# Kernel tuning notes

Hardware: AMD Instinct MI355X
Metric: run time of the kernel (lower is better)

The kernel has to match this reference:

```python
import jax, jax.numpy as jnp
import numpy as np

N = 50000      # nodes
E = 800000     # edges (avg degree 16)
F_IN = 64      # node_feature_dim
D = 128        # hidden_dim == output_dim
L = 3          # num_gnn_layers
B = 8          # number of graphs in the batch
GATE_H = 128   # GraphAttentionPool hidden_dim default


def _ln(x, g, b, eps=1e-5):
    m = x.mean(-1, keepdims=True)
    v = ((x - m) ** 2).mean(-1, keepdims=True)
    return (x - m) * jax.lax.rsqrt(v + eps) * g + b


def _gelu(x):
    return jax.nn.gelu(x, approximate=False)  # torch F.gelu default = exact erf


def setup_inputs() -> dict:
    key = jax.random.key(0)
    ks = jax.random.split(key, 12)
    p = lambda k, shape: (jax.random.normal(k, shape, jnp.float32) * 0.02)
    return {
        "x": jax.random.normal(ks[0], (N, F_IN), jnp.float32),
        "edge_index": jax.random.randint(ks[1], (2, E), 0, N, dtype=jnp.int32),
        "batch": jnp.sort(jax.random.randint(ks[2], (N,), 0, B, dtype=jnp.int32)),
        # input_proj: Linear + LayerNorm
        "w_in": p(ks[3], (F_IN, D)), "b_in": jnp.zeros((D,), jnp.float32),
        "ln_in_g": jnp.ones((D,), jnp.float32), "ln_in_b": jnp.zeros((D,), jnp.float32),
        # fallback GNN layers (stacked: all layers are 2D -> D)
        "gnn_w": p(ks[4], (L, 2 * D, D)), "gnn_b": jnp.zeros((L, D), jnp.float32),
        "gnn_ln_g": jnp.ones((L, D), jnp.float32), "gnn_ln_b": jnp.zeros((L, D), jnp.float32),
        # outer per-layer norms
        "norm_g": jnp.ones((L, D), jnp.float32), "norm_b": jnp.zeros((L, D), jnp.float32),
        # attention pool gate: Linear(D,128) -> tanh -> Linear(128,1)
        "gate_w1": p(ks[5], (D, GATE_H)), "gate_b1": jnp.zeros((GATE_H,), jnp.float32),
        "gate_w2": p(ks[6], (GATE_H,)), "gate_b2": jnp.zeros((), jnp.float32),
        # out_proj: Linear + LayerNorm + GELU
        "out_w": p(ks[7], (D, D)), "out_b": jnp.zeros((D,), jnp.float32),
        "out_ln_g": jnp.ones((D,), jnp.float32), "out_ln_b": jnp.zeros((D,), jnp.float32),
    }


def reference(x, edge_index, batch, w_in, b_in, ln_in_g, ln_in_b,
              gnn_w, gnn_b, gnn_ln_g, gnn_ln_b, norm_g, norm_b,
              gate_w1, gate_b1, gate_w2, gate_b2,
              out_w, out_b, out_ln_g, out_ln_b):
    src, dst = edge_index[0], edge_index[1]
    n = x.shape[0]

    # input_proj: Linear -> LayerNorm -> GELU
    h = _gelu(_ln(x @ w_in + b_in, ln_in_g, ln_in_b))

    # in-degree count (same every layer), clamped to >= 1
    deg = jax.ops.segment_sum(jnp.ones((src.shape[0],), h.dtype), dst, num_segments=n)
    deg = jnp.maximum(deg, 1.0)[:, None]  # (N, 1)

    for i in range(L):
        # mean-neighbor aggregation: gather x[src], scatter-add to dst
        agg = jax.ops.segment_sum(h[src], dst, num_segments=n) / deg  # (N, D)
        out = jnp.concatenate([h, agg], axis=-1) @ gnn_w[i] + gnn_b[i]
        h_new = _ln(_gelu(out), gnn_ln_g[i], gnn_ln_b[i])   # layer-internal norm
        h_new = _ln(h_new, norm_g[i], norm_b[i])             # outer norm
        if i < L - 1:
            h_new = _gelu(h_new) + h                         # residual (shapes match)
        h = h_new

    # attention pool (fallback path: global softmax over all nodes)
    gate_logits = jnp.tanh(h @ gate_w1 + gate_b1) @ gate_w2 + gate_b2  # (N,)
    gate = jax.nn.softmax(gate_logits, axis=0)
    pooled = jax.ops.segment_sum(h * gate[:, None], batch, num_segments=B)  # (B, D)

    spatial_embedding = _gelu(_ln(pooled @ out_w + out_b, out_ln_g, out_ln_b))
    return spatial_embedding, h, gate
```

## Files before the change

kernel.cpp:

```cpp
#include <hip/hip_runtime.h>
#include <math.h>

#define N_NODES 50000
#define N_EDGES 800000
#define F_IN 64
#define D 128
#define NLAYER 3
#define B_GRAPHS 8
#define GB 32
#define NPW 8
#define NBLK ((N_NODES + GB - 1) / GB)
#define SCAN_B 512
#define NPART ((N_NODES + SCAN_B - 1) / SCAN_B)
#define AGP 136

typedef float f32x4 __attribute__((ext_vector_type(4)));
typedef short bf16x8 __attribute__((ext_vector_type(8)));

__device__ __forceinline__ float gelu_exact(float x) {
    return 0.5f * x * (1.0f + erff(x * 0.7071067811865476f));
}

__device__ __forceinline__ unsigned short f2bf(float f) {
    unsigned int u = __float_as_uint(f);
    u = (u + 0x7fffu + ((u >> 16) & 1u)) >> 16;
    return (unsigned short)u;
}
__device__ __forceinline__ float bf2f(unsigned short u) {
    return __uint_as_float((unsigned int)u << 16);
}


__global__ void degree_kernel(const int* __restrict__ dst, int* __restrict__ deg) {
    int e = blockIdx.x * blockDim.x + threadIdx.x;
    if (e < N_EDGES) atomicAdd(&deg[dst[e]], 1);
}

__global__ __launch_bounds__(SCAN_B) void scan_partials_kernel(const int* __restrict__ deg,
                                                               int* __restrict__ partials) {
    __shared__ int wsum[8];
    int tid = threadIdx.x;
    int lane = tid & 63, wave = tid >> 6;
    int i = blockIdx.x * SCAN_B + tid;
    int v = (i < N_NODES) ? deg[i] : 0;
    #pragma unroll
    for (int o = 32; o >= 1; o >>= 1) v += __shfl_xor(v, o);
    if (lane == 0) wsum[wave] = v;
    __syncthreads();
    if (tid == 0) {
        int t = 0;
        #pragma unroll
        for (int w = 0; w < 8; ++w) t += wsum[w];
        partials[blockIdx.x] = t;
    }
}

__global__ __launch_bounds__(SCAN_B) void scan_apply_v2(const int* __restrict__ deg,
        const int* __restrict__ partials, int* __restrict__ row_ptr, int* __restrict__ cursor) {
    __shared__ int wsum[8];
    __shared__ int base_s;
    int tid = threadIdx.x;
    int lane = tid & 63, wave = tid >> 6;

    int b = 0;
    for (int i = tid; i < (int)blockIdx.x; i += SCAN_B) b += partials[i];
    #pragma unroll
    for (int o = 32; o >= 1; o >>= 1) b += __shfl_xor(b, o);
    if (lane == 0) wsum[wave] = b;
    __syncthreads();
    if (tid == 0) {
        int t = 0;
        #pragma unroll
        for (int w = 0; w < 8; ++w) t += wsum[w];
        base_s = t;
    }
    __syncthreads();
    int base = base_s;
    __syncthreads();

    if (blockIdx.x == 0) {
        int t = 0;
        for (int i = tid; i < NPART; i += SCAN_B) t += partials[i];
        #pragma unroll
        for (int o = 32; o >= 1; o >>= 1) t += __shfl_xor(t, o);
        if (lane == 0) wsum[wave] = t;
        __syncthreads();
        if (tid == 0) {
            int tt = 0;
            #pragma unroll
            for (int w = 0; w < 8; ++w) tt += wsum[w];
            row_ptr[N_NODES] = tt;
        }
        __syncthreads();
    }

    int i = blockIdx.x * SCAN_B + tid;
    int v = (i < N_NODES) ? deg[i] : 0;
    int x = v;
    #pragma unroll
    for (int o = 1; o < 64; o <<= 1) { int nb = __shfl_up(x, o); if (lane >= o) x += nb; }
    if (lane == 63) wsum[wave] = x;
    __syncthreads();
    int waveoff = 0;
    #pragma unroll
    for (int w = 0; w < 8; ++w) waveoff += (w < wave) ? wsum[w] : 0;
    int excl = base + waveoff + x - v;
    if (i < N_NODES) { row_ptr[i] = excl; cursor[i] = excl; }
}

__global__ void fill_kernel(const int* __restrict__ src, const int* __restrict__ dst,
                            int* __restrict__ cursor, int* __restrict__ csr) {
    int e = blockIdx.x * blockDim.x + threadIdx.x;
    if (e < N_EDGES) {
        int t = dst[e];
        int pos = atomicAdd(&cursor[t], 1);
        csr[pos] = src[e];
    }
}

#define WT_GNN (NLAYER * D * 2 * D)
#define WT_G1  (WT_GNN + D * D)
#define WT_ALL (WT_G1 + D * F_IN)
__global__ void wprep_kernel(const float* __restrict__ gnn_w, const float* __restrict__ gate_w1,
                             const float* __restrict__ w_in, unsigned short* __restrict__ wt,
                             float* __restrict__ pooled) {
    int idx = blockIdx.x * 256 + threadIdx.x;
    if (blockIdx.x == 0) {
        #pragma unroll
        for (int i = 0; i < 4; ++i) pooled[threadIdx.x + i * 256] = 0.f;
    }
    if (idx >= WT_ALL) return;
    if (idx < WT_GNN) {
        int l = idx / (D * 2 * D);
        int rem = idx - l * (D * 2 * D);
        int n = rem / (2 * D);
        int k = rem - n * (2 * D);
        wt[idx] = f2bf(gnn_w[(size_t)l * 2 * D * D + (size_t)k * D + n]);
    } else if (idx < WT_G1) {
        int rem = idx - WT_GNN;
        int n = rem / D;
        int k = rem - n * D;
        wt[idx] = f2bf(gate_w1[(size_t)k * D + n]);
    } else {
        int rem = idx - WT_G1;
        int n = rem / F_IN;
        int k = rem - n * F_IN;
        wt[idx] = f2bf(w_in[(size_t)k * D + n]);
    }
}


__global__ __launch_bounds__(256) void input_proj_v5(
        const float* __restrict__ x, const unsigned short* __restrict__ wti,
        const float* __restrict__ b, const float* __restrict__ gam,
        const float* __restrict__ bet, unsigned short* __restrict__ h16) {
    __shared__ float2 red[2][GB];
    int tid = threadIdx.x;
    int wave = tid >> 6, lane = tid & 63;
    int nblk0 = blockIdx.x * GB;
    int q = lane >> 4, c = lane & 15;
    int m0 = (wave >> 1) * 16;
    int n0 = (wave & 1) * 64;
    int mrow = nblk0 + m0 + c;
    int mclamp = (mrow < N_NODES) ? mrow : (N_NODES - 1);
    const float* xr = x + (size_t)mclamp * F_IN;

    f32x4 acc[4];
    #pragma unroll
    for (int t = 0; t < 4; ++t) {
        float bn = b[n0 + t * 16 + c];
        acc[t] = (f32x4){bn, bn, bn, bn};
    }
    #pragma unroll
    for (int kk = 0; kk < 2; ++kk) {
        float4 a0 = *(const float4*)&xr[kk * 32 + q * 8];
        float4 a1 = *(const float4*)&xr[kk * 32 + q * 8 + 4];
        bf16x8 av;
        av[0] = (short)f2bf(a0.x); av[1] = (short)f2bf(a0.y);
        av[2] = (short)f2bf(a0.z); av[3] = (short)f2bf(a0.w);
        av[4] = (short)f2bf(a1.x); av[5] = (short)f2bf(a1.y);
        av[6] = (short)f2bf(a1.z); av[7] = (short)f2bf(a1.w);
        #pragma unroll
        for (int t = 0; t < 4; ++t) {
            bf16x8 bv = *(const bf16x8*)&wti[(size_t)(n0 + t * 16 + c) * F_IN + kk * 32 + q * 8];
            acc[t] = __builtin_amdgcn_mfma_f32_16x16x32_bf16(av, bv, acc[t], 0, 0, 0);
        }
    }
    float s[4], sq[4];
    #pragma unroll
    for (int r = 0; r < 4; ++r) {
        s[r] = acc[0][r] + acc[1][r] + acc[2][r] + acc[3][r];
        sq[r] = acc[0][r] * acc[0][r] + acc[1][r] * acc[1][r]
              + acc[2][r] * acc[2][r] + acc[3][r] * acc[3][r];
    }
    #pragma unroll
    for (int o = 1; o <= 8; o <<= 1)
        #pragma unroll
        for (int r = 0; r < 4; ++r) { s[r] += __shfl_xor(s[r], o); sq[r] += __shfl_xor(sq[r], o); }
    if (c == 0) {
        #pragma unroll
        for (int r = 0; r < 4; ++r) red[wave & 1][m0 + q * 4 + r] = make_float2(s[r], sq[r]);
    }
    __syncthreads();
    float gv[4], bv2[4];
    #pragma unroll
    for (int t = 0; t < 4; ++t) {
        int nn = n0 + t * 16 + c;
        gv[t] = gam[nn]; bv2[t] = bet[nn];
    }
    #pragma unroll
    for (int r = 0; r < 4; ++r) {
        int m = m0 + q * 4 + r;
        int n = nblk0 + m;
        float2 p0 = red[0][m], p1 = red[1][m];
        float mean = (p0.x + p1.x) * (1.0f / D);
        float msq  = (p0.y + p1.y) * (1.0f / D);
        float istd = rsqrtf(msq - mean * mean + 1e-5f);
        if (n < N_NODES) {
            #pragma unroll
            for (int t = 0; t < 4; ++t) {
                int nn = n0 + t * 16 + c;
                float y = (acc[t][r] - mean) * istd * gv[t] + bv2[t];
                h16[(size_t)n * D + nn] = f2bf(gelu_exact(y));
            }
        }
    }
}


__device__ __forceinline__ void acc_row(float acc[8], bf16x8 v) {
    #pragma unroll
    for (int i = 0; i < 8; ++i)
        acc[i] += __uint_as_float(((unsigned int)(unsigned short)v[i]) << 16);
}

template<int DO_GATE>
__global__ __launch_bounds__(256) void gnn_layer_v8(
        const unsigned short* __restrict__ h16_in, unsigned short* __restrict__ h16_out,
        float* __restrict__ hf_out,
        const int* __restrict__ csr, const int* __restrict__ rp,
        const unsigned short* __restrict__ wt,
        const float* __restrict__ bias,
        const float* __restrict__ ln1g, const float* __restrict__ ln1b,
        const float* __restrict__ ln2g, const float* __restrict__ ln2b,
        int residual, int write_f32,
        const unsigned short* __restrict__ wtg,
        const float* __restrict__ gb1, const float* __restrict__ gw2,
        const float* __restrict__ gb2,
        float* __restrict__ logits, float2* __restrict__ gpart) {
    __shared__ int rps[GB + 1];
    __shared__ int eidx[GB][32];
    __shared__ unsigned short aggb[GB][AGP];
    __shared__ float2 red1[2][GB];
    __shared__ float2 red2[2][GB];
    __shared__ float redg[2][GB];
    __shared__ float lg[GB];

    int tid = threadIdx.x;
    int wave = tid >> 6, lane = tid & 63;
    int nblk0 = blockIdx.x * GB;
    int gbase = wave * NPW;

    if (tid < GB + 1) {
        int n = nblk0 + tid;
        if (n > N_NODES) n = N_NODES;
        rps[tid] = rp[n];
    }
    __syncthreads();
    #pragma unroll
    for (int k2 = 0; k2 < 4; ++k2) {
        int f = tid + k2 * 256;
        int g = f >> 5, sl = f & 31;
        int beg = rps[g], end = rps[g + 1];
        int ee = beg + sl;
        int ci = (ee < end) ? ee : ((end > beg) ? (end - 1) : 0);
        eidx[g][sl] = csr[ci];
    }
    __syncthreads();

    {
        int er = lane >> 4, dg = lane & 15;
        #pragma unroll
        for (int jj = 0; jj < NPW; jj += 2) {
            int gA = gbase + jj, gB2 = gbase + jj + 1;
            int begA = rps[gA], endA = rps[gA + 1];
            int begB = rps[gB2], endB = rps[gB2 + 1];
            int degA = endA - begA, degB = endB - begB;
            int idA[8], idB[8];
            #pragma unroll
            for (int t = 0; t < 8; ++t) { idA[t] = eidx[gA][er + 4 * t]; idB[t] = eidx[gB2][er + 4 * t]; }
            bf16x8 vA[8], vB[8];
            #pragma unroll
            for (int t = 0; t < 8; ++t)
                vA[t] = *(const bf16x8*)&h16_in[(size_t)idA[t] * D + dg * 8];
            #pragma unroll
            for (int t = 0; t < 8; ++t)
                vB[t] = *(const bf16x8*)&h16_in[(size_t)idB[t] * D + dg * 8];

            float accA[8], accB[8];
            #pragma unroll
            for (int i = 0; i < 8; ++i) { accA[i] = 0.f; accB[i] = 0.f; }
            #pragma unroll
            for (int t = 0; t < 8; ++t)
                if (begA + er + 4 * t < endA) acc_row(accA, vA[t]);
            #pragma unroll
            for (int t = 0; t < 8; ++t)
                if (begB + er + 4 * t < endB) acc_row(accB, vB[t]);
            if (degA > 32) {
                for (int ee = begA + er + 32; ee < endA; ee += 4) {
                    bf16x8 vv = *(const bf16x8*)&h16_in[(size_t)csr[ee] * D + dg * 8];
                    acc_row(accA, vv);
                }
            }
            if (degB > 32) {
                for (int ee = begB + er + 32; ee < endB; ee += 4) {
                    bf16x8 vv = *(const bf16x8*)&h16_in[(size_t)csr[ee] * D + dg * 8];
                    acc_row(accB, vv);
                }
            }
            #pragma unroll
            for (int i = 0; i < 8; ++i) {
                accA[i] += __shfl_xor(accA[i], 16);
                accA[i] += __shfl_xor(accA[i], 32);
                accB[i] += __shfl_xor(accB[i], 16);
                accB[i] += __shfl_xor(accB[i], 32);
            }
            float invA = 1.0f / fmaxf((float)degA, 1.0f);
            float invB = 1.0f / fmaxf((float)degB, 1.0f);
            if (er == 0) {
                bf16x8 oA, oB;
                #pragma unroll
                for (int i = 0; i < 8; ++i) {
                    oA[i] = (short)f2bf(accA[i] * invA);
                    oB[i] = (short)f2bf(accB[i] * invB);
                }
                *(bf16x8*)&aggb[gA][dg * 8] = oA;
                *(bf16x8*)&aggb[gB2][dg * 8] = oB;
            }
        }
    }
    __syncthreads();

    int q = lane >> 4, c = lane & 15;
    int m0 = (wave >> 1) * 16;
    int n0 = (wave & 1) * 64;
    int mrow = nblk0 + m0 + c;
    int mclamp = (mrow < N_NODES) ? mrow : (N_NODES - 1);
    const unsigned short* arow = h16_in + (size_t)mclamp * D;

    f32x4 acc[4];
    #pragma unroll
    for (int t = 0; t < 4; ++t) {
        float bn = bias[n0 + t * 16 + c];
        acc[t] = (f32x4){bn, bn, bn, bn};
    }
    #pragma unroll
    for (int kk = 0; kk < 4; ++kk) {
        bf16x8 av = *(const bf16x8*)&arow[kk * 32 + q * 8];
        #pragma unroll
        for (int t = 0; t < 4; ++t) {
            bf16x8 bv = *(const bf16x8*)&wt[(size_t)(n0 + t * 16 + c) * 256 + kk * 32 + q * 8];
            acc[t] = __builtin_amdgcn_mfma_f32_16x16x32_bf16(av, bv, acc[t], 0, 0, 0);
        }
    }
    #pragma unroll
    for (int kk = 0; kk < 4; ++kk) {
        bf16x8 av = *(const bf16x8*)&aggb[m0 + c][kk * 32 + q * 8];
        #pragma unroll
        for (int t = 0; t < 4; ++t) {
            bf16x8 bv = *(const bf16x8*)&wt[(size_t)(n0 + t * 16 + c) * 256 + 128 + kk * 32 + q * 8];
            acc[t] = __builtin_amdgcn_mfma_f32_16x16x32_bf16(av, bv, acc[t], 0, 0, 0);
        }
    }

    float xv[4][4];
    #pragma unroll
    for (int t = 0; t < 4; ++t)
        #pragma unroll
        for (int r = 0; r < 4; ++r) xv[t][r] = gelu_exact(acc[t][r]);

    float s[4], sq[4];
    #pragma unroll
    for (int r = 0; r < 4; ++r) {
        s[r] = xv[0][r] + xv[1][r] + xv[2][r] + xv[3][r];
        sq[r] = xv[0][r] * xv[0][r] + xv[1][r] * xv[1][r] + xv[2][r] * xv[2][r] + xv[3][r] * xv[3][r];
    }
    #pragma unroll
    for (int o = 1; o <= 8; o <<= 1)
        #pragma unroll
        for (int r = 0; r < 4; ++r) { s[r] += __shfl_xor(s[r], o); sq[r] += __shfl_xor(sq[r], o); }
    int nh = wave & 1;
    if (c == 0) {
        #pragma unroll
        for (int r = 0; r < 4; ++r) red1[nh][m0 + q * 4 + r] = make_float2(s[r], sq[r]);
    }
    __syncthreads();

    float g1v[4], b1v[4], g2v[4], b2v[4];
    #pragma unroll
    for (int t = 0; t < 4; ++t) {
        int nn = n0 + t * 16 + c;
        g1v[t] = ln1g[nn]; b1v[t] = ln1b[nn];
        g2v[t] = ln2g[nn]; b2v[t] = ln2b[nn];
    }

    float y1[4][4];
    #pragma unroll
    for (int r = 0; r < 4; ++r) {
        int m = m0 + q * 4 + r;
        float2 p0 = red1[0][m], p1 = red1[1][m];
        float mean = (p0.x + p1.x) * (1.0f / D);
        float msq  = (p0.y + p1.y) * (1.0f / D);
        float istd = rsqrtf(msq - mean * mean + 1e-5f);
        #pragma unroll
        for (int t = 0; t < 4; ++t)
            y1[t][r] = (xv[t][r] - mean) * istd * g1v[t] + b1v[t];
    }

    #pragma unroll
    for (int r = 0; r < 4; ++r) {
        s[r] = y1[0][r] + y1[1][r] + y1[2][r] + y1[3][r];
        sq[r] = y1[0][r] * y1[0][r] + y1[1][r] * y1[1][r] + y1[2][r] * y1[2][r] + y1[3][r] * y1[3][r];
    }
    #pragma unroll
    for (int o = 1; o <= 8; o <<= 1)
        #pragma unroll
        for (int r = 0; r < 4; ++r) { s[r] += __shfl_xor(s[r], o); sq[r] += __shfl_xor(sq[r], o); }
    if (c == 0) {
        #pragma unroll
        for (int r = 0; r < 4; ++r) red2[nh][m0 + q * 4 + r] = make_float2(s[r], sq[r]);
    }
    __syncthreads();

    #pragma unroll
    for (int r = 0; r < 4; ++r) {
        int m = m0 + q * 4 + r;
        int n = nblk0 + m;
        float2 p0 = red2[0][m], p1 = red2[1][m];
        float mean = (p0.x + p1.x) * (1.0f / D);
        float msq  = (p0.y + p1.y) * (1.0f / D);
        float istd = rsqrtf(msq - mean * mean + 1e-5f);
        #pragma unroll
        for (int t = 0; t < 4; ++t) {
            int nn = n0 + t * 16 + c;
            float y2 = (y1[t][r] - mean) * istd * g2v[t] + b2v[t];
            float o = residual ? (gelu_exact(y2) + bf2f(h16_in[(size_t)n * D + nn])) : y2;
            if (n < N_NODES) {
                h16_out[(size_t)n * D + nn] = f2bf(o);
                if (write_f32) hf_out[(size_t)n * D + nn] = o;
            }
            if (DO_GATE) aggb[m][nn] = f2bf(o);
        }
    }

    if (DO_GATE) {
        __syncthreads();
        f32x4 gacc[4];
        #pragma unroll
        for (int t = 0; t < 4; ++t) {
            float bn = gb1[n0 + t * 16 + c];
            gacc[t] = (f32x4){bn, bn, bn, bn};
        }
        #pragma unroll
        for (int kk = 0; kk < 4; ++kk) {
            bf16x8 av = *(const bf16x8*)&aggb[m0 + c][kk * 32 + q * 8];
            #pragma unroll
            for (int t = 0; t < 4; ++t) {
                bf16x8 bv = *(const bf16x8*)&wtg[(size_t)(n0 + t * 16 + c) * 128 + kk * 32 + q * 8];
                gacc[t] = __builtin_amdgcn_mfma_f32_16x16x32_bf16(av, bv, gacc[t], 0, 0, 0);
            }
        }
        float w2v[4];
        #pragma unroll
        for (int t = 0; t < 4; ++t) w2v[t] = gw2[n0 + t * 16 + c];
        float gs[4];
        #pragma unroll
        for (int r = 0; r < 4; ++r) {
            gs[r] = tanhf(gacc[0][r]) * w2v[0] + tanhf(gacc[1][r]) * w2v[1]
                  + tanhf(gacc[2][r]) * w2v[2] + tanhf(gacc[3][r]) * w2v[3];
        }
        #pragma unroll
        for (int o = 1; o <= 8; o <<= 1)
            #pragma unroll
            for (int r = 0; r < 4; ++r) gs[r] += __shfl_xor(gs[r], o);
        if (c == 0) {
            #pragma unroll
            for (int r = 0; r < 4; ++r) redg[nh][m0 + q * 4 + r] = gs[r];
        }
        __syncthreads();
        if ((wave & 1) == 0 && c == 0) {
            float bb2 = gb2[0];
            #pragma unroll
            for (int r = 0; r < 4; ++r) {
                int m = m0 + q * 4 + r;
                int n = nblk0 + m;
                float L = redg[0][m] + redg[1][m] + bb2;
                if (n < N_NODES) { logits[n] = L; lg[m] = L; }
                else lg[m] = -INFINITY;
            }
        }
        __syncthreads();
        if (wave == 0) {
            float l = (lane < GB) ? lg[lane] : -INFINITY;
            float mx = l;
            #pragma unroll
            for (int o = 32; o >= 1; o >>= 1) mx = fmaxf(mx, __shfl_xor(mx, o));
            float ex = (lane < GB && l > -INFINITY) ? expf(l - mx) : 0.f;
            #pragma unroll
            for (int o = 32; o >= 1; o >>= 1) ex += __shfl_xor(ex, o);
            if (lane == 0) gpart[blockIdx.x] = make_float2(mx, ex);
        }
    }
}


#define PC 64
__global__ __launch_bounds__(128) void gate_pool_v3(
        const unsigned short* __restrict__ h16, const float* __restrict__ logits,
        const float2* __restrict__ gpart, const int* __restrict__ batch,
        float* __restrict__ gate_out, float* __restrict__ pooled) {
    __shared__ float sb[4];
    __shared__ float gs[PC];
    __shared__ int bs[PC];
    int d = threadIdx.x;
    int lane = d & 63, wv = d >> 6;
    float mx = -INFINITY;
    for (int i = d; i < NBLK; i += 128) mx = fmaxf(mx, gpart[i].x);
    #pragma unroll
    for (int o = 32; o >= 1; o >>= 1) mx = fmaxf(mx, __shfl_xor(mx, o));
    if (lane == 0) sb[wv] = mx;
    __syncthreads();
    mx = fmaxf(sb[0], sb[1]);
    float ssum = 0.f;
    for (int i = d; i < NBLK; i += 128) {
        float2 p = gpart[i];
        ssum += p.y * expf(p.x - mx);
    }
    #pragma unroll
    for (int o = 32; o >= 1; o >>= 1) ssum += __shfl_xor(ssum, o);
    if (lane == 0) sb[2 + wv] = ssum;
    __syncthreads();
    float inv = 1.0f / (sb[2] + sb[3]);

    int n0 = blockIdx.x * PC;
    if (d < PC) {
        int nj = n0 + d;
        if (nj < N_NODES) {
            float gv = expf(logits[nj] - mx) * inv;
            gs[d] = gv;
            bs[d] = batch[nj];
            gate_out[nj] = gv;
        }
    }
    __syncthreads();
    int count = min(PC, N_NODES - n0);
    float acc = 0.f;
    int cur = bs[0];
    int t = 0;
    for (; t + 3 < count; t += 4) {
        float h0 = bf2f(h16[(size_t)(n0 + t + 0) * D + d]);
        float h1 = bf2f(h16[(size_t)(n0 + t + 1) * D + d]);
        float h2 = bf2f(h16[(size_t)(n0 + t + 2) * D + d]);
        float h3 = bf2f(h16[(size_t)(n0 + t + 3) * D + d]);
        int b0 = bs[t], b1 = bs[t + 1], b2 = bs[t + 2], b3 = bs[t + 3];
        if (b0 != cur) { atomicAdd(&pooled[cur * D + d], acc); acc = 0.f; cur = b0; }
        acc = fmaf(h0, gs[t], acc);
        if (b1 != cur) { atomicAdd(&pooled[cur * D + d], acc); acc = 0.f; cur = b1; }
        acc = fmaf(h1, gs[t + 1], acc);
        if (b2 != cur) { atomicAdd(&pooled[cur * D + d], acc); acc = 0.f; cur = b2; }
        acc = fmaf(h2, gs[t + 2], acc);
        if (b3 != cur) { atomicAdd(&pooled[cur * D + d], acc); acc = 0.f; cur = b3; }
        acc = fmaf(h3, gs[t + 3], acc);
    }
    for (; t < count; ++t) {
        int bn = bs[t];
        if (bn != cur) { atomicAdd(&pooled[cur * D + d], acc); acc = 0.f; cur = bn; }
        acc = fmaf(bf2f(h16[(size_t)(n0 + t) * D + d]), gs[t], acc);
    }
    atomicAdd(&pooled[cur * D + d], acc);
}

__global__ void out_proj_kernel(const float* __restrict__ pooled, const float* __restrict__ w,
                                const float* __restrict__ b, const float* __restrict__ g,
                                const float* __restrict__ beta, float* __restrict__ emb) {
    __shared__ float ps[D];
    __shared__ float sbuf[2];
    int bg = blockIdx.x, d = threadIdx.x;
    ps[d] = pooled[bg * D + d];
    __syncthreads();
    float acc = b[d];
    #pragma unroll 8
    for (int k = 0; k < D; ++k) acc += ps[k] * w[k * D + d];
    float s = acc, q = acc * acc;
    #pragma unroll
    for (int o = 32; o >= 1; o >>= 1) { s += __shfl_down(s, o); q += __shfl_down(q, o); }
    if ((d & 63) == 0) { sbuf[d >> 6] = s; }
    __syncthreads();
    float fullsum = sbuf[0] + sbuf[1];
    __syncthreads();
    if ((d & 63) == 0) { sbuf[d >> 6] = q; }
    __syncthreads();
    float fullsq = sbuf[0] + sbuf[1];
    float m = fullsum * (1.0f / D);
    float var = fullsq * (1.0f / D) - m * m;
    float y = (acc - m) * rsqrtf(var + 1e-5f) * g[d] + beta[d];
    emb[bg * D + d] = gelu_exact(y);
}

extern "C" void kernel_launch(void* const* d_in, const int* in_sizes, int n_in,
                              void* d_out, int out_size, void* d_ws, size_t ws_size,
                              hipStream_t stream) {
    const float* x        = (const float*)d_in[0];
    const int*   edge     = (const int*)d_in[1];
    const int*   batch    = (const int*)d_in[2];
    const float* w_in     = (const float*)d_in[3];
    const float* b_in     = (const float*)d_in[4];
    const float* ln_in_g  = (const float*)d_in[5];
    const float* ln_in_b  = (const float*)d_in[6];
    const float* gnn_w    = (const float*)d_in[7];
    const float* gnn_b    = (const float*)d_in[8];
    const float* gnn_ln_g = (const float*)d_in[9];
    const float* gnn_ln_b = (const float*)d_in[10];
    const float* norm_g   = (const float*)d_in[11];
    const float* norm_b   = (const float*)d_in[12];
    const float* gate_w1  = (const float*)d_in[13];
    const float* gate_b1  = (const float*)d_in[14];
    const float* gate_w2  = (const float*)d_in[15];
    const float* gate_b2  = (const float*)d_in[16];
    const float* out_w    = (const float*)d_in[17];
    const float* out_b    = (const float*)d_in[18];
    const float* out_ln_g = (const float*)d_in[19];
    const float* out_ln_b = (const float*)d_in[20];

    const int* src = edge;
    const int* dst = edge + N_EDGES;

    float* out      = (float*)d_out;
    float* emb      = out;
    float* hA       = out + B_GRAPHS * D;
    float* gate_out = hA + (size_t)N_NODES * D;

    unsigned short* h16A = (unsigned short*)d_ws;
    unsigned short* h16B = h16A + (size_t)N_NODES * D;
    int*   deg_i    = (int*)d_ws;
    int*   cursor   = (int*)d_ws + N_NODES;
    int*   row_ptr  = (int*)(h16B + (size_t)N_NODES * D);
    int*   csr      = row_ptr + N_NODES + 1;
    float* logits   = (float*)(csr + N_EDGES);
    float* pooled   = logits + N_NODES;
    int*   partials = (int*)(pooled + B_GRAPHS * D);
    float2* gpart   = (float2*)(((uintptr_t)(partials + NPART) + 15) & ~(uintptr_t)15);
    unsigned short* wt  = (unsigned short*)(gpart + NBLK);
    unsigned short* wtg = wt + WT_GNN;
    unsigned short* wti = wt + WT_G1;

    hipMemsetAsync(deg_i, 0, N_NODES * sizeof(int), stream);
    degree_kernel<<<(N_EDGES + 255) / 256, 256, 0, stream>>>(dst, deg_i);
    scan_partials_kernel<<<NPART, SCAN_B, 0, stream>>>(deg_i, partials);
    scan_apply_v2<<<NPART, SCAN_B, 0, stream>>>(deg_i, partials, row_ptr, cursor);
    fill_kernel<<<(N_EDGES + 255) / 256, 256, 0, stream>>>(src, dst, cursor, csr);
    wprep_kernel<<<(WT_ALL + 255) / 256, 256, 0, stream>>>(gnn_w, gate_w1, w_in, wt, pooled);

    input_proj_v5<<<NBLK, 256, 0, stream>>>(x, wti, b_in, ln_in_g, ln_in_b, h16B);

    gnn_layer_v8<0><<<NBLK, 256, 0, stream>>>(
        h16B, h16A, hA, csr, row_ptr, wt, gnn_b,
        gnn_ln_g, gnn_ln_b, norm_g, norm_b, 1, 0,
        nullptr, nullptr, nullptr, nullptr, nullptr, nullptr);
    gnn_layer_v8<0><<<NBLK, 256, 0, stream>>>(
        h16A, h16B, hA, csr, row_ptr, wt + (size_t)1 * D * 2 * D, gnn_b + D,
        gnn_ln_g + D, gnn_ln_b + D, norm_g + D, norm_b + D, 1, 0,
        nullptr, nullptr, nullptr, nullptr, nullptr, nullptr);
    gnn_layer_v8<1><<<NBLK, 256, 0, stream>>>(
        h16B, h16A, hA, csr, row_ptr, wt + (size_t)2 * D * 2 * D, gnn_b + 2 * D,
        gnn_ln_g + 2 * D, gnn_ln_b + 2 * D, norm_g + 2 * D, norm_b + 2 * D, 0, 1,
        wtg, gate_b1, gate_w2, gate_b2, logits, gpart);

    gate_pool_v3<<<(N_NODES + PC - 1) / PC, 128, 0, stream>>>(
        h16A, logits, gpart, batch, gate_out, pooled);
    out_proj_kernel<<<B_GRAPHS, D, 0, stream>>>(pooled, out_w, out_b, out_ln_g, out_ln_b, emb);
}
```

Before: 458.8 us.

## Make GNN layer wave-independent: each wave owns 16 nodes and full 128-column GEMM

Restructures the GNN layer kernel so each wave handles 16 nodes end to end: it builds its own edge index list, gathers neighbours, and computes all 128 output columns with MFMA, keeping the LayerNorm reductions inside the wave. This removes most block-level __syncthreads and the shared-memory partial reductions across waves. Blocks now cover 64 nodes, and the gather uses a 16-edge fast path with a second batch only when degree exceeds 16. In exchange each wave uses more registers (8 accumulator tiles) and streams the whole weight matrix, which may reduce occupancy.

```diff
diff --git a/kernel.cpp b/kernel.cpp
--- a/kernel.cpp
+++ b/kernel.cpp
@@ -8,8 +8,10 @@
 #define NLAYER 3
 #define B_GRAPHS 8
 #define GB 32
-#define NPW 8
 #define NBLK ((N_NODES + GB - 1) / GB)
+#define WNODE 16
+#define GB2 64
+#define NBLK2 ((N_NODES + GB2 - 1) / GB2)
 #define SCAN_B 512
 #define NPART ((N_NODES + SCAN_B - 1) / SCAN_B)
 #define AGP 136
@@ -235,7 +237,7 @@
 }
 
 template<int DO_GATE>
-__global__ __launch_bounds__(256) void gnn_layer_v8(
+__global__ __launch_bounds__(256) void gnn_layer_v9(
         const unsigned short* __restrict__ h16_in, unsigned short* __restrict__ h16_out,
         float* __restrict__ hf_out,
         const int* __restrict__ csr, const int* __restrict__ rp,
@@ -248,264 +250,250 @@
         const float* __restrict__ gb1, const float* __restrict__ gw2,
         const float* __restrict__ gb2,
         float* __restrict__ logits, float2* __restrict__ gpart) {
-    __shared__ int rps[GB + 1];
-    __shared__ int eidx[GB][32];
-    __shared__ unsigned short aggb[GB][AGP];
-    __shared__ float2 red1[2][GB];
-    __shared__ float2 red2[2][GB];
-    __shared__ float redg[2][GB];
-    __shared__ float lg[GB];
+    __shared__ int rps[4][WNODE + 1];
+    __shared__ int eidx[4][WNODE][32];
+    __shared__ unsigned short aggb[4][WNODE][AGP];
+    __shared__ float lg[GB2];
 
     int tid = threadIdx.x;
     int wave = tid >> 6, lane = tid & 63;
-    int nblk0 = blockIdx.x * GB;
-    int gbase = wave * NPW;
-
-    if (tid < GB + 1) {
-        int n = nblk0 + tid;
+    int nw0 = blockIdx.x * GB2 + wave * WNODE;
+    int er = lane >> 4, dg = lane & 15;
+
+    if (lane < WNODE + 1) {
+        int n = nw0 + lane;
         if (n > N_NODES) n = N_NODES;
-        rps[tid] = rp[n];
-    }
-    __syncthreads();
-    #pragma unroll
-    for (int k2 = 0; k2 < 4; ++k2) {
-        int f = tid + k2 * 256;
-        int g = f >> 5, sl = f & 31;
-        int beg = rps[g], end = rps[g + 1];
+        rps[wave][lane] = rp[n];
+    }
+    #pragma unroll
+    for (int it = 0; it < 8; ++it) {
+        int j = it * 2 + (lane >> 5);
+        int sl = lane & 31;
+        int beg = rps[wave][j], end = rps[wave][j + 1];
         int ee = beg + sl;
         int ci = (ee < end) ? ee : ((end > beg) ? (end - 1) : 0);
-        eidx[g][sl] = csr[ci];
-    }
-    __syncthreads();
-
-    {
-        int er = lane >> 4, dg = lane & 15;
-        #pragma unroll
-        for (int jj = 0; jj < NPW; jj += 2) {
-            int gA = gbase + jj, gB2 = gbase + jj + 1;
-            int begA = rps[gA], endA = rps[gA + 1];
-            int begB = rps[gB2], endB = rps[gB2 + 1];
-            int degA = endA - begA, degB = endB - begB;
-            int idA[8], idB[8];
-            #pragma unroll
-            for (int t = 0; t < 8; ++t) { idA[t] = eidx[gA][er + 4 * t]; idB[t] = eidx[gB2][er + 4 * t]; }
-            bf16x8 vA[8], vB[8];
-            #pragma unroll
-            for (int t = 0; t < 8; ++t)
-                vA[t] = *(const bf16x8*)&h16_in[(size_t)idA[t] * D + dg * 8];
-            #pragma unroll
-            for (int t = 0; t < 8; ++t)
-                vB[t] = *(const bf16x8*)&h16_in[(size_t)idB[t] * D + dg * 8];
-
-            float accA[8], accB[8];
-            #pragma unroll
-            for (int i = 0; i < 8; ++i) { accA[i] = 0.f; accB[i] = 0.f; }
-            #pragma unroll
-            for (int t = 0; t < 8; ++t)
-                if (begA + er + 4 * t < endA) acc_row(accA, vA[t]);
-            #pragma unroll
-            for (int t = 0; t < 8; ++t)
-                if (begB + er + 4 * t < endB) acc_row(accB, vB[t]);
-            if (degA > 32) {
+        eidx[wave][j][sl] = csr[ci];
+    }
+
+    #pragma unroll
+    for (int jj = 0; jj < WNODE; jj += 2) {
+        int begA = rps[wave][jj], endA = rps[wave][jj + 1];
+        int begB = endA, endB = rps[wave][jj + 2];
+        int degA = endA - begA, degB = endB - begB;
+        int idA[4], idB[4];
+        #pragma unroll
+        for (int t = 0; t < 4; ++t) {
+            idA[t] = eidx[wave][jj][er + 4 * t];
+            idB[t] = eidx[wave][jj + 1][er + 4 * t];
+        }
+        bf16x8 vA[4], vB[4];
+        #pragma unroll
+        for (int t = 0; t < 4; ++t)
+            vA[t] = *(const bf16x8*)&h16_in[(size_t)idA[t] * D + dg * 8];
+        #pragma unroll
+        for (int t = 0; t < 4; ++t)
+            vB[t] = *(const bf16x8*)&h16_in[(size_t)idB[t] * D + dg * 8];
+        float accA[8], accB[8];
+        #pragma unroll
+        for (int i = 0; i < 8; ++i) { accA[i] = 0.f; accB[i] = 0.f; }
+        #pragma unroll
+        for (int t = 0; t < 4; ++t) {
+            if (begA + er + 4 * t < endA) acc_row(accA, vA[t]);
+            if (begB + er + 4 * t < endB) acc_row(accB, vB[t]);
+        }
+        if (degA > 16 || degB > 16) {
+            int idA2[4], idB2[4];
+            #pragma unroll
+            for (int t = 0; t < 4; ++t) {
+                idA2[t] = eidx[wave][jj][16 + er + 4 * t];
+                idB2[t] = eidx[wave][jj + 1][16 + er + 4 * t];
+            }
+            bf16x8 wA[4], wB[4];
+            #pragma unroll
+            for (int t = 0; t < 4; ++t)
+                wA[t] = *(const bf16x8*)&h16_in[(size_t)idA2[t] * D + dg * 8];
+            #pragma unroll
+            for (int t = 0; t < 4; ++t)
+                wB[t] = *(const bf16x8*)&h16_in[(size_t)idB2[t] * D + dg * 8];
+            #pragma unroll
+            for (int t = 0; t < 4; ++t) {
+                if (begA + 16 + er + 4 * t < endA) acc_row(accA, wA[t]);
+                if (begB + 16 + er + 4 * t < endB) acc_row(accB, wB[t]);
+            }
+            if (degA > 32)
                 for (int ee = begA + er + 32; ee < endA; ee += 4) {
                     bf16x8 vv = *(const bf16x8*)&h16_in[(size_t)csr[ee] * D + dg * 8];
                     acc_row(accA, vv);
                 }
-            }
-            if (degB > 32) {
+            if (degB > 32)
                 for (int ee = begB + er + 32; ee < endB; ee += 4) {
                     bf16x8 vv = *(const bf16x8*)&h16_in[(size_t)csr[ee] * D + dg * 8];
                     acc_row(accB, vv);
                 }
+        }
+        #pragma unroll
+        for (int i = 0; i < 8; ++i) {
+            accA[i] += __shfl_xor(accA[i], 16);
+            accA[i] += __shfl_xor(accA[i], 32);
+            accB[i] += __shfl_xor(accB[i], 16);
+            accB[i] += __shfl_xor(accB[i], 32);
+        }
+        float invA = 1.0f / fmaxf((float)degA, 1.0f);
+        float invB = 1.0f / fmaxf((float)degB, 1.0f);
+        if (er == 0) {
+            bf16x8 oA, oB;
+            #pragma unroll
+            for (int i = 0; i < 8; ++i) {
+                oA[i] = (short)f2bf(accA[i] * invA);
+                oB[i] = (short)f2bf(accB[i] * invB);
             }
-            #pragma unroll
-            for (int i = 0; i < 8; ++i) {
-                accA[i] += __shfl_xor(accA[i], 16);
-                accA[i] += __shfl_xor(accA[i], 32);
-                accB[i] += __shfl_xor(accB[i], 16);
-                accB[i] += __shfl_xor(accB[i], 32);
-            }
-            float invA = 1.0f / fmaxf((float)degA, 1.0f);
-            float invB = 1.0f / fmaxf((float)degB, 1.0f);
-            if (er == 0) {
-                bf16x8 oA, oB;
-                #pragma unroll
-                for (int i = 0; i < 8; ++i) {
-                    oA[i] = (short)f2bf(accA[i] * invA);
-                    oB[i] = (short)f2bf(accB[i] * invB);
-                }
-                *(bf16x8*)&aggb[gA][dg * 8] = oA;
-                *(bf16x8*)&aggb[gB2][dg * 8] = oB;
-            }
-        }
-    }
-    __syncthreads();
+            *(bf16x8*)&aggb[wave][jj][dg * 8] = oA;
+            *(bf16x8*)&aggb[wave][jj + 1][dg * 8] = oB;
+        }
+    }
 
     int q = lane >> 4, c = lane & 15;
-    int m0 = (wave >> 1) * 16;
-    int n0 = (wave & 1) * 64;
-    int mrow = nblk0 + m0 + c;
+    int mrow = nw0 + c;
     int mclamp = (mrow < N_NODES) ? mrow : (N_NODES - 1);
     const unsigned short* arow = h16_in + (size_t)mclamp * D;
 
-    f32x4 acc[4];
-    #pragma unroll
-    for (int t = 0; t < 4; ++t) {
-        float bn = bias[n0 + t * 16 + c];
+    f32x4 acc[8];
+    #pragma unroll
+    for (int t = 0; t < 8; ++t) {
+        float bn = bias[t * 16 + c];
         acc[t] = (f32x4){bn, bn, bn, bn};
     }
     #pragma unroll
     for (int kk = 0; kk < 4; ++kk) {
         bf16x8 av = *(const bf16x8*)&arow[kk * 32 + q * 8];
         #pragma unroll
-        for (int t = 0; t < 4; ++t) {
-            bf16x8 bv = *(const bf16x8*)&wt[(size_t)(n0 + t * 16 + c) * 256 + kk * 32 + q * 8];
+        for (int t = 0; t < 8; ++t) {
+            bf16x8 bv = *(const bf16x8*)&wt[(size_t)(t * 16 + c) * 256 + kk * 32 + q * 8];
             acc[t] = __builtin_amdgcn_mfma_f32_16x16x32_bf16(av, bv, acc[t], 0, 0, 0);
         }
     }
     #pragma unroll
     for (int kk = 0; kk < 4; ++kk) {
-        bf16x8 av = *(const bf16x8*)&aggb[m0 + c][kk * 32 + q * 8];
-        #pragma unroll
-        for (int t = 0; t < 4; ++t) {
-            bf16x8 bv = *(const bf16x8*)&wt[(size_t)(n0 + t * 16 + c) * 256 + 128 + kk * 32 + q * 8];
+        bf16x8 av = *(const bf16x8*)&aggb[wave][c][kk * 32 + q * 8];
+        #pragma unroll
+        for (int t = 0; t < 8; ++t) {
+            bf16x8 bv = *(const bf16x8*)&wt[(size_t)(t * 16 + c) * 256 + 128 + kk * 32 + q * 8];
             acc[t] = __builtin_amdgcn_mfma_f32_16x16x32_bf16(av, bv, acc[t], 0, 0, 0);
         }
     }
 
-    float xv[4][4];
-    #pragma unroll
-    for (int t = 0; t < 4; ++t)
+    float xv[8][4];
+    #pragma unroll
+    for (int t = 0; t < 8; ++t)
         #pragma unroll
         for (int r = 0; r < 4; ++r) xv[t][r] = gelu_exact(acc[t][r]);
 
     float s[4], sq[4];
     #pragma unroll
     for (int r = 0; r < 4; ++r) {
-        s[r] = xv[0][r] + xv[1][r] + xv[2][r] + xv[3][r];
-        sq[r] = xv[0][r] * xv[0][r] + xv[1][r] * xv[1][r] + xv[2][r] * xv[2][r] + xv[3][r] * xv[3][r];
+        s[r] = 0.f; sq[r] = 0.f;
+        #pragma unroll
+        for (int t = 0; t < 8; ++t) { s[r] += xv[t][r]; sq[r] += xv[t][r] * xv[t][r]; }
     }
     #pragma unroll
     for (int o = 1; o <= 8; o <<= 1)
         #pragma unroll
         for (int r = 0; r < 4; ++r) { s[r] += __shfl_xor(s[r], o); sq[r] += __shfl_xor(sq[r], o); }
-    int nh = wave & 1;
-    if (c == 0) {
-        #pragma unroll
-        for (int r = 0; r < 4; ++r) red1[nh][m0 + q * 4 + r] = make_float2(s[r], sq[r]);
-    }
-    __syncthreads();
-
-    float g1v[4], b1v[4], g2v[4], b2v[4];
-    #pragma unroll
-    for (int t = 0; t < 4; ++t) {
-        int nn = n0 + t * 16 + c;
+
+    float g1v[8], b1v[8], g2v[8], b2v[8];
+    #pragma unroll
+    for (int t = 0; t < 8; ++t) {
+        int nn = t * 16 + c;
         g1v[t] = ln1g[nn]; b1v[t] = ln1b[nn];
         g2v[t] = ln2g[nn]; b2v[t] = ln2b[nn];
     }
 
-    float y1[4][4];
+    float y1[8][4];
+    float s2[4], sq2[4];
     #pragma unroll
     for (int r = 0; r < 4; ++r) {
-        int m = m0 + q * 4 + r;
-        float2 p0 = red1[0][m], p1 = red1[1][m];
-        float mean = (p0.x + p1.x) * (1.0f / D);
-        float msq  = (p0.y + p1.y) * (1.0f / D);
+        float mean = s[r] * (1.0f / D);
+        float msq  = sq[r] * (1.0f / D);
         float istd = rsqrtf(msq - mean * mean + 1e-5f);
-        #pragma unroll
-        for (int t = 0; t < 4; ++t)
-            y1[t][r] = (xv[t][r] - mean) * istd * g1v[t] + b1v[t];
-    }
+        s2[r] = 0.f; sq2[r] = 0.f;
+        #pragma unroll
+        for (int t = 0; t < 8; ++t) {
+            float y = (xv[t][r] - mean) * istd * g1v[t] + b1v[t];
+            y1[t][r] = y;
+            s2[r] += y; sq2[r] += y * y;
+        }
+    }
+    #pragma unroll
+    for (int o = 1; o <= 8; o <<= 1)
+        #pragma unroll
+        for (int r = 0; r < 4; ++r) { s2[r] += __shfl_xor(s2[r], o); sq2[r] += __shfl_xor(sq2[r], o); }
 
     #pragma unroll
     for (int r = 0; r < 4; ++r) {
-        s[r] = y1[0][r] + y1[1][r] + y1[2][r] + y1[3][r];
-        sq[r] = y1[0][r] * y1[0][r] + y1[1][r] * y1[1][r] + y1[2][r] * y1[2][r] + y1[3][r] * y1[3][r];
-    }
-    #pragma unroll
-    for (int o = 1; o <= 8; o <<= 1)
-        #pragma unroll
-        for (int r = 0; r < 4; ++r) { s[r] += __shfl_xor(s[r], o); sq[r] += __shfl_xor(sq[r], o); }
-    if (c == 0) {
-        #pragma unroll
-        for (int r = 0; r < 4; ++r) red2[nh][m0 + q * 4 + r] = make_float2(s[r], sq[r]);
-    }
-    __syncthreads();
-
-    #pragma unroll
-    for (int r = 0; r < 4; ++r) {
-        int m = m0 + q * 4 + r;
-        int n = nblk0 + m;
-        float2 p0 = red2[0][m], p1 = red2[1][m];
-        float mean = (p0.x + p1.x) * (1.0f / D);
-        float msq  = (p0.y + p1.y) * (1.0f / D);
+        int m = q * 4 + r;
+        int n = nw0 + m;
+        float mean = s2[r] * (1.0f / D);
+        float msq  = sq2[r] * (1.0f / D);
         float istd = rsqrtf(msq - mean * mean + 1e-5f);
         #pragma unroll
-        for (int t = 0; t < 4; ++t) {
-            int nn = n0 + t * 16 + c;
+        for (int t = 0; t < 8; ++t) {
+            int nn = t * 16 + c;
             float y2 = (y1[t][r] - mean) * istd * g2v[t] + b2v[t];
             float o = residual ? (gelu_exact(y2) + bf2f(h16_in[(size_t)n * D + nn])) : y2;
             if (n < N_NODES) {
                 h16_out[(size_t)n * D + nn] = f2bf(o);
                 if (write_f32) hf_out[(size_t)n * D + nn] = o;
             }
-            if (DO_GATE) aggb[m][nn] = f2bf(o);
+            if (DO_GATE) aggb[wave][m][nn] = f2bf(o);
         }
     }
 
     if (DO_GATE) {
-        __syncthreads();
-        f32x4 gacc[4];
-        #pragma unroll
-        for (int t = 0; t < 4; ++t) {
-            float bn = gb1[n0 + t * 16 + c];
+        f32x4 gacc[8];
+        #pragma unroll
+        for (int t = 0; t < 8; ++t) {
+            float bn = gb1[t * 16 + c];
             gacc[t] = (f32x4){bn, bn, bn, bn};
         }
         #pragma unroll
         for (int kk = 0; kk < 4; ++kk) {
-            bf16x8 av = *(const bf16x8*)&aggb[m0 + c][kk * 32 + q * 8];
-            #pragma unroll
-            for (int t = 0; t < 4; ++t) {
-                bf16x8 bv = *(const bf16x8*)&wtg[(size_t)(n0 + t * 16 + c) * 128 + kk * 32 + q * 8];
+            bf16x8 av = *(const bf16x8*)&aggb[wave][c][kk * 32 + q * 8];
+            #pragma unroll
+            for (int t = 0; t < 8; ++t) {
+                bf16x8 bv = *(const bf16x8*)&wtg[(size_t)(t * 16 + c) * 128 + kk * 32 + q * 8];
                 gacc[t] = __builtin_amdgcn_mfma_f32_16x16x32_bf16(av, bv, gacc[t], 0, 0, 0);
             }
         }
-        float w2v[4];
-        #pragma unroll
-        for (int t = 0; t < 4; ++t) w2v[t] = gw2[n0 + t * 16 + c];
         float gs[4];
         #pragma unroll
         for (int r = 0; r < 4; ++r) {
-            gs[r] = tanhf(gacc[0][r]) * w2v[0] + tanhf(gacc[1][r]) * w2v[1]
-                  + tanhf(gacc[2][r]) * w2v[2] + tanhf(gacc[3][r]) * w2v[3];
+            gs[r] = 0.f;
+            #pragma unroll
+            for (int t = 0; t < 8; ++t)
+                gs[r] += tanhf(gacc[t][r]) * gw2[t * 16 + c];
         }
         #pragma unroll
         for (int o = 1; o <= 8; o <<= 1)
             #pragma unroll
             for (int r = 0; r < 4; ++r) gs[r] += __shfl_xor(gs[r], o);
         if (c == 0) {
-            #pragma unroll
-            for (int r = 0; r < 4; ++r) redg[nh][m0 + q * 4 + r] = gs[r];
-        }
-        __syncthreads();
-        if ((wave & 1) == 0 && c == 0) {
             float bb2 = gb2[0];
             #pragma unroll
             for (int r = 0; r < 4; ++r) {
-                int m = m0 + q * 4 + r;
-                int n = nblk0 + m;
-                float L = redg[0][m] + redg[1][m] + bb2;
-                if (n < N_NODES) { logits[n] = L; lg[m] = L; }
-                else lg[m] = -INFINITY;
+                int m = q * 4 + r;
+                int n = nw0 + m;
+                float L = gs[r] + bb2;
+                if (n < N_NODES) { logits[n] = L; lg[wave * WNODE + m] = L; }
+                else lg[wave * WNODE + m] = -INFINITY;
             }
         }
         __syncthreads();
         if (wave == 0) {
-            float l = (lane < GB) ? lg[lane] : -INFINITY;
+            float l = lg[lane];
             float mx = l;
             #pragma unroll
             for (int o = 32; o >= 1; o >>= 1) mx = fmaxf(mx, __shfl_xor(mx, o));
-            float ex = (lane < GB && l > -INFINITY) ? expf(l - mx) : 0.f;
+            float ex = (l > -INFINITY) ? expf(l - mx) : 0.f;
             #pragma unroll
             for (int o = 32; o >= 1; o >>= 1) ex += __shfl_xor(ex, o);
             if (lane == 0) gpart[blockIdx.x] = make_float2(mx, ex);
@@ -525,14 +513,14 @@
     int d = threadIdx.x;
     int lane = d & 63, wv = d >> 6;
     float mx = -INFINITY;
-    for (int i = d; i < NBLK; i += 128) mx = fmaxf(mx, gpart[i].x);
+    for (int i = d; i < NBLK2; i += 128) mx = fmaxf(mx, gpart[i].x);
     #pragma unroll
     for (int o = 32; o >= 1; o >>= 1) mx = fmaxf(mx, __shfl_xor(mx, o));
     if (lane == 0) sb[wv] = mx;
     __syncthreads();
     mx = fmaxf(sb[0], sb[1]);
     float ssum = 0.f;
-    for (int i = d; i < NBLK; i += 128) {
+    for (int i = d; i < NBLK2; i += 128) {
         float2 p = gpart[i];
         ssum += p.y * expf(p.x - mx);
     }
@@ -650,7 +638,7 @@
     float* pooled   = logits + N_NODES;
     int*   partials = (int*)(pooled + B_GRAPHS * D);
     float2* gpart   = (float2*)(((uintptr_t)(partials + NPART) + 15) & ~(uintptr_t)15);
-    unsigned short* wt  = (unsigned short*)(gpart + NBLK);
+    unsigned short* wt  = (unsigned short*)(gpart + NBLK2);
     unsigned short* wtg = wt + WT_GNN;
     unsigned short* wti = wt + WT_G1;
 
@@ -663,15 +651,15 @@
 
     input_proj_v5<<<NBLK, 256, 0, stream>>>(x, wti, b_in, ln_in_g, ln_in_b, h16B);
 
-    gnn_layer_v8<0><<<NBLK, 256, 0, stream>>>(
+    gnn_layer_v9<0><<<NBLK2, 256, 0, stream>>>(
         h16B, h16A, hA, csr, row_ptr, wt, gnn_b,
         gnn_ln_g, gnn_ln_b, norm_g, norm_b, 1, 0,
         nullptr, nullptr, nullptr, nullptr, nullptr, nullptr);
-    gnn_layer_v8<0><<<NBLK, 256, 0, stream>>>(
+    gnn_layer_v9<0><<<NBLK2, 256, 0, stream>>>(
         h16A, h16B, hA, csr, row_ptr, wt + (size_t)1 * D * 2 * D, gnn_b + D,
         gnn_ln_g + D, gnn_ln_b + D, norm_g + D, norm_b + D, 1, 0,
         nullptr, nullptr, nullptr, nullptr, nullptr, nullptr);
-    gnn_layer_v8<1><<<NBLK, 256, 0, stream>>>(
+    gnn_layer_v9<1><<<NBLK2, 256, 0, stream>>>(
         h16B, h16A, hA, csr, row_ptr, wt + (size_t)2 * D * 2 * D, gnn_b + 2 * D,
         gnn_ln_g + 2 * D, gnn_ln_b + 2 * D, norm_g + 2 * D, norm_b + 2 * D, 0, 1,
         wtg, gate_b1, gate_w2, gate_b2, logits, gpart);
```

Result: slower. 503.4 us (+9.7%).
